# Kernel optimization log

Measured on AMD Instinct MI355X. Metric: run time of the kernel, lower is better.

Reference implementation:

```python
import jax, jax.numpy as jnp
import numpy as np

ITEM_NUM = 100000
EMBED = 128
HIDDEN = 256
BETA = 0.5
B, H = 2048, 200


def setup_inputs() -> dict:
    key = jax.random.key(0)
    ks = jax.random.split(key, 10)
    history = jax.random.randint(ks[0], (B, H), 0, ITEM_NUM)
    target = jax.random.randint(ks[1], (B,), 0, ITEM_NUM)
    history_region = jax.random.randint(ks[2], (B, H), 0, 64)
    target_region = jax.random.randint(ks[3], (B,), 0, 64)
    # scaled small since forward multiplies by 1000 before sigmoid
    target_distance = jax.random.uniform(ks[4], (B, H, 2), dtype=jnp.float32) * 1e-3
    embed_history = 0.01 * jax.random.normal(ks[5], (ITEM_NUM, EMBED), dtype=jnp.float32)
    embed_target = 0.01 * jax.random.normal(ks[6], (ITEM_NUM, EMBED), dtype=jnp.float32)
    W1 = 0.05 * jax.random.normal(ks[7], (EMBED + 2, HIDDEN), dtype=jnp.float32)
    b1 = jnp.zeros((HIDDEN,), dtype=jnp.float32)
    W2 = 0.05 * jax.random.normal(ks[8], (HIDDEN, 1), dtype=jnp.float32)
    Wd = 0.5 * jax.random.normal(ks[9], (2, 2), dtype=jnp.float32)
    bd = jnp.zeros((2,), dtype=jnp.float32)
    return {"history": history, "target": target, "history_region": history_region,
            "target_region": target_region, "target_distance": target_distance,
            "embed_history": embed_history, "embed_target": embed_target,
            "W1": W1, "b1": b1, "W2": W2, "Wd": Wd, "bd": bd}


def reference(history, target, history_region, target_region, target_distance,
              embed_history, embed_target, W1, b1, W2, Wd, bd):
    h = embed_history[history]                 # [B,H,d]
    t = embed_target[target]                   # [B,d]
    # dist_layer: sigmoid(Linear(2,2)(1000 * lat_long))
    dist = jax.nn.sigmoid((target_distance * 1000.0) @ Wd + bd)   # [B,H,2]
    inp = jnp.concatenate([h * t[:, None, :], dist], axis=-1)     # [B,H,d+2]
    attn = jax.nn.relu(inp @ W1 + b1) @ W2                        # [B,H,1]
    mask = (history != target[:, None]).astype(h.dtype)
    exp_A = jnp.exp(attn[..., 0]) * mask                          # [B,H]
    exp_sum = jnp.sum(exp_A, axis=-1, keepdims=True) ** BETA      # [B,1]
    w = exp_A / exp_sum                                           # [B,H]
    pred = jnp.einsum('bhd,bh,bd->b', h, w, t)                    # [B]
    return jax.nn.sigmoid(pred)
```

## Files before the change

kernel.cpp:

```cpp
#include <hip/hip_runtime.h>
#include <hip/hip_bf16.h>

#define B_SZ 2048
#define H_SZ 200
#define EMB 128
#define HID 256
#define KW 160

typedef short bf16x8 __attribute__((ext_vector_type(8)));
typedef float f32x4 __attribute__((ext_vector_type(4)));

#define WAIT_VM(n) asm volatile("s_waitcnt vmcnt(" #n ")" ::: "memory")
#define WAIT_LGKM  asm volatile("s_waitcnt lgkmcnt(0)" ::: "memory")
#define BAR        asm volatile("s_barrier" ::: "memory")

__device__ __forceinline__ unsigned short bfc(float x) {
    unsigned u = __float_as_uint(x);
    u += 0x7FFFu + ((u >> 16) & 1u);
    return (unsigned short)(u >> 16);
}
__device__ __forceinline__ float bf2f(unsigned short h) {
    return __uint_as_float(((unsigned)h) << 16);
}

__global__ void prep_w1t(const float* __restrict__ W1, unsigned short* __restrict__ W1TB) {
    int i = blockIdx.x * 256 + threadIdx.x;
    int n = i / KW;
    int k = i - n * KW;
    float v = (k < 130) ? W1[k * HID + n] : 0.f;
    W1TB[i] = bfc(v);
}

__global__ void prep_ehb(const float* __restrict__ eh, unsigned short* __restrict__ ehb) {
    size_t t = (size_t)blockIdx.x * 256 + threadIdx.x;
    const float4* src = (const float4*)eh + t * 2;
    float4 a = src[0], b = src[1];
    uint4 o;
    o.x = (unsigned)bfc(a.x) | ((unsigned)bfc(a.y) << 16);
    o.y = (unsigned)bfc(a.z) | ((unsigned)bfc(a.w) << 16);
    o.z = (unsigned)bfc(b.x) | ((unsigned)bfc(b.y) << 16);
    o.w = (unsigned)bfc(b.z) | ((unsigned)bfc(b.w) << 16);
    ((uint4*)ehb)[t] = o;
}

__device__ __forceinline__ void gld_lds16(const unsigned short* g, unsigned short* l) {
    __builtin_amdgcn_global_load_lds(
        (const __attribute__((address_space(1))) void*)(g),
        (__attribute__((address_space(3))) void*)(l),
        16, 0, 0);
}

__global__ __launch_bounds__(512, 4) void attn_kernel(
    const int* __restrict__ history, const int* __restrict__ target,
    const float* __restrict__ td, const unsigned short* __restrict__ ehb,
    const float* __restrict__ et, const unsigned short* __restrict__ W1TB,
    const float* __restrict__ b1, const float* __restrict__ W2,
    const float* __restrict__ Wd, const float* __restrict__ bd,
    float* __restrict__ out)
{
    __shared__ __align__(16) unsigned short Abuf[4][64][128];
    __shared__ float red[4][64][9];
    __shared__ unsigned Adist[256];
    __shared__ int idxs[256];
    __shared__ float t_f32[EMB];
    __shared__ __align__(16) unsigned short tbf[EMB];
    __shared__ float u_arr[256];
    __shared__ float finred[8];

    const int tid = threadIdx.x;
    const int b   = blockIdx.x;
    const int tgt = target[b];

    if (tid < 128) {
        float tf = et[(size_t)tgt * EMB + tid];
        t_f32[tid] = tf;
        tbf[tid] = bfc(tf);
    } else if (tid < 384) {
        const int m0 = tid - 128;
        if (m0 < H_SZ) {
            const int row = b * H_SZ + m0;
            idxs[m0] = history[row];
            float x0 = td[(size_t)row * 2 + 0] * 1000.f;
            float x1 = td[(size_t)row * 2 + 1] * 1000.f;
            float d0 = x0 * Wd[0] + x1 * Wd[2] + bd[0];
            float d1 = x0 * Wd[1] + x1 * Wd[3] + bd[1];
            d0 = 1.f / (1.f + expf(-d0));
            d1 = 1.f / (1.f + expf(-d1));
            Adist[m0] = (unsigned)bfc(d0) | ((unsigned)bfc(d1) << 16);
        } else {
            Adist[m0] = 0u;
        }
    }
    WAIT_LGKM; BAR;

    const int l  = tid & 63;
    const int w  = tid >> 6;
    const int lr = l & 15;
    const int lq = l >> 4;

    bf16x8 bfrA[2][5];
    f32x4 b1v[2], w2v[2];
#pragma unroll
    for (int nt = 0; nt < 2; ++nt) {
        const int n = w * 32 + nt * 16 + lr;
        b1v[nt] = *reinterpret_cast<const f32x4*>(b1 + w * 32 + nt * 16 + lq * 4);
        w2v[nt] = *reinterpret_cast<const f32x4*>(W2 + w * 32 + nt * 16 + lq * 4);
#pragma unroll
        for (int ks = 0; ks < 4; ++ks) {
            bf16x8 wv = *reinterpret_cast<const bf16x8*>(W1TB + n * KW + ks * 32 + lq * 8);
            bf16x8 o;
#pragma unroll
            for (int j = 0; j < 8; ++j)
                o[j] = (short)bfc(bf2f((unsigned short)wv[j]) * t_f32[ks * 32 + lq * 8 + j]);
            bfrA[nt][ks] = o;
        }
        bfrA[nt][4] = *reinterpret_cast<const bf16x8*>(W1TB + n * KW + 128 + lq * 8);
    }

    const int uo = tid & 7, um = tid >> 3;
    const bf16x8 tbu0 = *reinterpret_cast<const bf16x8*>(tbf + (2 * uo) * 8);
    const bf16x8 tbu1 = *reinterpret_cast<const bf16x8*>(tbf + (2 * uo + 1) * 8);

    WAIT_VM(0);

#pragma unroll
    for (int t = 0; t < 3; ++t) {
#pragma unroll
        for (int j = 0; j < 2; ++j) {
            const int rd = w * 8 + j * 4 + lq;
            const int cc = lr ^ (rd & 7);
            gld_lds16(ehb + (size_t)idxs[t * 64 + rd] * EMB + cc * 8,
                      &Abuf[t][w * 8 + j * 4][0]);
        }
    }
    if (w < 2) {
        const int rd = w * 4 + lq;
        const int cc = lr ^ (rd & 7);
        gld_lds16(ehb + (size_t)idxs[192 + rd] * EMB + cc * 8, &Abuf[3][w * 4][0]);
    }

#pragma unroll
    for (int t = 0; t < 4; ++t) {
        if (t == 0)      { if (w < 2) WAIT_VM(5); else WAIT_VM(4); }
        else if (t == 1) { if (w < 2) WAIT_VM(3); else WAIT_VM(2); }
        else if (t == 2) { if (w < 2) WAIT_VM(1); else WAIT_VM(0); }
        else             WAIT_VM(0);
        BAR;

        const int mc = (t == 3) ? 1 : 4;

        f32x4 acc[4][2];
#pragma unroll
        for (int mt = 0; mt < 4; ++mt)
#pragma unroll
            for (int nt = 0; nt < 2; ++nt)
                acc[mt][nt] = (f32x4){0.f, 0.f, 0.f, 0.f};

#pragma unroll
        for (int ks = 0; ks < 5; ++ks) {
#pragma unroll
            for (int mt = 0; mt < 4; ++mt) if (mt < mc) {
                const int ar = mt * 16 + lr;
                bf16x8 af;
                if (ks < 4) {
                    af = *reinterpret_cast<const bf16x8*>(
                        &Abuf[t][ar][(((ks * 4 + lq) ^ (ar & 7)) * 8)]);
                } else {
                    uint4 tv4 = make_uint4((lq == 0) ? Adist[t * 64 + ar] : 0u, 0u, 0u, 0u);
                    af = *reinterpret_cast<bf16x8*>(&tv4);
                }
#pragma unroll
                for (int nt = 0; nt < 2; ++nt)
                    acc[mt][nt] = __builtin_amdgcn_mfma_f32_16x16x32_bf16(
                        bfrA[nt][ks], af, acc[mt][nt], 0, 0, 0);
            }
        }

        {
            const unsigned short* Ar = &Abuf[t][um][0];
            bf16x8 h0 = *reinterpret_cast<const bf16x8*>(Ar + (((2 * uo)     ^ (um & 7)) * 8));
            bf16x8 h1 = *reinterpret_cast<const bf16x8*>(Ar + (((2 * uo + 1) ^ (um & 7)) * 8));
            float ua = 0.f;
#pragma unroll
            for (int j = 0; j < 8; ++j) {
                ua += bf2f((unsigned short)h0[j]) * bf2f((unsigned short)tbu0[j]);
                ua += bf2f((unsigned short)h1[j]) * bf2f((unsigned short)tbu1[j]);
            }
            ua += __shfl_xor(ua, 1);
            ua += __shfl_xor(ua, 2);
            ua += __shfl_xor(ua, 4);
            if (uo == 0) u_arr[t * 64 + um] = ua;
        }

#pragma unroll
        for (int mt = 0; mt < 4; ++mt) if (mt < mc) {
            float s = 0.f;
#pragma unroll
            for (int nt = 0; nt < 2; ++nt)
#pragma unroll
                for (int r = 0; r < 4; ++r)
                    s += fmaxf(acc[mt][nt][r] + b1v[nt][r], 0.f) * w2v[nt][r];
            s += __shfl_xor(s, 16);
            s += __shfl_xor(s, 32);
            if (l < 16) red[t][mt * 16 + l][w] = s;
        }
    }

    WAIT_LGKM; BAR;

    if (tid < 256) {
        const int tt = tid >> 6, mr = tid & 63;
        float attn = 0.f;
#pragma unroll
        for (int ww = 0; ww < 8; ++ww) attn += red[tt][mr][ww];
        const bool valid = (tid < H_SZ) && (idxs[tid] != tgt);
        float e  = valid ? expf(attn) : 0.f;
        float se = e;
        float su = valid ? e * u_arr[tid] : 0.f;
#pragma unroll
        for (int off = 1; off < 64; off <<= 1) {
            se += __shfl_xor(se, off);
            su += __shfl_xor(su, off);
        }
        if (l == 0) { finred[w * 2] = se; finred[w * 2 + 1] = su; }
    }
    WAIT_LGKM; BAR;
    if (tid == 0) {
        float SE = 0.f, SU = 0.f;
#pragma unroll
        for (int ww = 0; ww < 4; ++ww) { SE += finred[2 * ww]; SU += finred[2 * ww + 1]; }
        out[b] = 1.f / (1.f + expf(-SU / sqrtf(SE)));
    }
}

extern "C" void kernel_launch(void* const* d_in, const int* in_sizes, int n_in,
                              void* d_out, int out_size, void* d_ws, size_t ws_size,
                              hipStream_t stream) {
    const int*   history = (const int*)d_in[0];
    const int*   target  = (const int*)d_in[1];
    const float* td      = (const float*)d_in[4];
    const float* eh      = (const float*)d_in[5];
    const float* et      = (const float*)d_in[6];
    const float* W1      = (const float*)d_in[7];
    const float* b1      = (const float*)d_in[8];
    const float* W2      = (const float*)d_in[9];
    const float* Wd      = (const float*)d_in[10];
    const float* bd      = (const float*)d_in[11];
    float* out = (float*)d_out;

    char* ws = (char*)d_ws;
    unsigned short* W1TB = (unsigned short*)ws;
    unsigned short* ehb  = (unsigned short*)(ws + 81920);

    prep_w1t<<<HID * KW / 256, 256, 0, stream>>>(W1, W1TB);
    prep_ehb<<<1600000 / 256, 256, 0, stream>>>(eh, ehb);
    attn_kernel<<<B_SZ, 512, 0, stream>>>(history, target, td, ehb, et, W1TB,
                                          b1, W2, Wd, bd, out);
}
```

Before: 120.7 us.

## Double-buffer history tiles in LDS and fold softmax reduction into tile loop

Shrinks the shared-memory staging of gathered history rows from four tiles to two ping-pong buffers. Loads for tiles 2 and 3 are issued after earlier tiles are consumed, and the per-tile exp/weighted sums are accumulated inside the loop instead of in a separate final pass. Launch bounds are raised to allow more resident blocks per CU, using the smaller LDS footprint to hide gather latency through occupancy. The cost is an extra barrier per tile, less prefetch depth, and a tighter register budget that could cause spills.

```diff
diff --git a/kernel.cpp b/kernel.cpp
--- a/kernel.cpp
+++ b/kernel.cpp
@@ -50,7 +50,7 @@
         16, 0, 0);
 }
 
-__global__ __launch_bounds__(512, 4) void attn_kernel(
+__global__ __launch_bounds__(512, 8) void attn_kernel(
     const int* __restrict__ history, const int* __restrict__ target,
     const float* __restrict__ td, const unsigned short* __restrict__ ehb,
     const float* __restrict__ et, const unsigned short* __restrict__ W1TB,
@@ -58,14 +58,13 @@
     const float* __restrict__ Wd, const float* __restrict__ bd,
     float* __restrict__ out)
 {
-    __shared__ __align__(16) unsigned short Abuf[4][64][128];
-    __shared__ float red[4][64][9];
+    __shared__ __align__(16) unsigned short Abuf[2][64][128];
+    __shared__ float red[64][9];
     __shared__ unsigned Adist[256];
     __shared__ int idxs[256];
     __shared__ float t_f32[EMB];
     __shared__ __align__(16) unsigned short tbf[EMB];
-    __shared__ float u_arr[256];
-    __shared__ float finred[8];
+    __shared__ float u_t[64];
 
     const int tid = threadIdx.x;
     const int b   = blockIdx.x;
@@ -124,7 +123,7 @@
     WAIT_VM(0);
 
 #pragma unroll
-    for (int t = 0; t < 3; ++t) {
+    for (int t = 0; t < 2; ++t) {
 #pragma unroll
         for (int j = 0; j < 2; ++j) {
             const int rd = w * 8 + j * 4 + lq;
@@ -133,20 +132,18 @@
                       &Abuf[t][w * 8 + j * 4][0]);
         }
     }
-    if (w < 2) {
-        const int rd = w * 4 + lq;
-        const int cc = lr ^ (rd & 7);
-        gld_lds16(ehb + (size_t)idxs[192 + rd] * EMB + cc * 8, &Abuf[3][w * 4][0]);
-    }
+
+    float se = 0.f, su = 0.f;
 
 #pragma unroll
     for (int t = 0; t < 4; ++t) {
-        if (t == 0)      { if (w < 2) WAIT_VM(5); else WAIT_VM(4); }
-        else if (t == 1) { if (w < 2) WAIT_VM(3); else WAIT_VM(2); }
+        if (t == 0)      WAIT_VM(2);
+        else if (t == 1) WAIT_VM(2);
         else if (t == 2) { if (w < 2) WAIT_VM(1); else WAIT_VM(0); }
         else             WAIT_VM(0);
         BAR;
 
+        const int bi = t & 1;
         const int mc = (t == 3) ? 1 : 4;
 
         f32x4 acc[4][2];
@@ -164,7 +161,7 @@
                 bf16x8 af;
                 if (ks < 4) {
                     af = *reinterpret_cast<const bf16x8*>(
-                        &Abuf[t][ar][(((ks * 4 + lq) ^ (ar & 7)) * 8)]);
+                        &Abuf[bi][ar][(((ks * 4 + lq) ^ (ar & 7)) * 8)]);
                 } else {
                     uint4 tv4 = make_uint4((lq == 0) ? Adist[t * 64 + ar] : 0u, 0u, 0u, 0u);
                     af = *reinterpret_cast<bf16x8*>(&tv4);
@@ -177,7 +174,7 @@
         }
 
         {
-            const unsigned short* Ar = &Abuf[t][um][0];
+            const unsigned short* Ar = &Abuf[bi][um][0];
             bf16x8 h0 = *reinterpret_cast<const bf16x8*>(Ar + (((2 * uo)     ^ (um & 7)) * 8));
             bf16x8 h1 = *reinterpret_cast<const bf16x8*>(Ar + (((2 * uo + 1) ^ (um & 7)) * 8));
             float ua = 0.f;
@@ -189,7 +186,7 @@
             ua += __shfl_xor(ua, 1);
             ua += __shfl_xor(ua, 2);
             ua += __shfl_xor(ua, 4);
-            if (uo == 0) u_arr[t * 64 + um] = ua;
+            if (uo == 0) u_t[um] = ua;
         }
 
 #pragma unroll
@@ -202,34 +199,47 @@
                     s += fmaxf(acc[mt][nt][r] + b1v[nt][r], 0.f) * w2v[nt][r];
             s += __shfl_xor(s, 16);
             s += __shfl_xor(s, 32);
-            if (l < 16) red[t][mt * 16 + l][w] = s;
-        }
-    }
-
-    WAIT_LGKM; BAR;
-
-    if (tid < 256) {
-        const int tt = tid >> 6, mr = tid & 63;
-        float attn = 0.f;
-#pragma unroll
-        for (int ww = 0; ww < 8; ++ww) attn += red[tt][mr][ww];
-        const bool valid = (tid < H_SZ) && (idxs[tid] != tgt);
-        float e  = valid ? expf(attn) : 0.f;
-        float se = e;
-        float su = valid ? e * u_arr[tid] : 0.f;
+            if (l < 16) red[mt * 16 + l][w] = s;
+        }
+
+        WAIT_LGKM; BAR;
+
+        if (t == 0) {
+#pragma unroll
+            for (int j = 0; j < 2; ++j) {
+                const int rd = w * 8 + j * 4 + lq;
+                const int cc = lr ^ (rd & 7);
+                gld_lds16(ehb + (size_t)idxs[128 + rd] * EMB + cc * 8,
+                          &Abuf[0][w * 8 + j * 4][0]);
+            }
+        } else if (t == 1) {
+            if (w < 2) {
+                const int rd = w * 4 + lq;
+                const int cc = lr ^ (rd & 7);
+                gld_lds16(ehb + (size_t)idxs[192 + rd] * EMB + cc * 8,
+                          &Abuf[1][w * 4][0]);
+            }
+        }
+
+        if (tid < 64) {
+            const int grow = t * 64 + tid;
+            float attn = 0.f;
+#pragma unroll
+            for (int ww = 0; ww < 8; ++ww) attn += red[tid][ww];
+            const bool valid = (grow < H_SZ) && (idxs[grow] != tgt);
+            float e = valid ? expf(attn) : 0.f;
+            se += e;
+            su += valid ? e * u_t[tid] : 0.f;
+        }
+    }
+
+    if (tid < 64) {
 #pragma unroll
         for (int off = 1; off < 64; off <<= 1) {
             se += __shfl_xor(se, off);
             su += __shfl_xor(su, off);
         }
-        if (l == 0) { finred[w * 2] = se; finred[w * 2 + 1] = su; }
-    }
-    WAIT_LGKM; BAR;
-    if (tid == 0) {
-        float SE = 0.f, SU = 0.f;
-#pragma unroll
-        for (int ww = 0; ww < 4; ++ww) { SE += finred[2 * ww]; SU += finred[2 * ww + 1]; }
-        out[b] = 1.f / (1.f + expf(-SU / sqrtf(SE)));
+        if (tid == 0) out[b] = 1.f / (1.f + expf(-su / sqrtf(se)));
     }
 }
 
```

New measurement: 424.3 us. 251% more time.

## Load gathered history rows directly into registers with double-buffered 16-row tiles

Applied to the files above, without the earlier changes.

Drops the LDS staging of gathered embedding rows via global_load_lds. Each wave now loads its MFMA B-fragments for 16-row tiles straight from global memory into registers, double-buffered across 13 tiles, and the u dot product is computed from those registers by one rotating wave. This removes the 64KB LDS buffer and its barriers, but every wave now redundantly gathers the same rows (8x global/L2 traffic). The per-tile loop also has less MFMA work to hide load latency behind.

```diff
diff --git a/kernel.cpp b/kernel.cpp
--- a/kernel.cpp
+++ b/kernel.cpp
@@ -6,13 +6,10 @@
 #define EMB 128
 #define HID 256
 #define KW 160
+#define NTILE 13
 
 typedef short bf16x8 __attribute__((ext_vector_type(8)));
 typedef float f32x4 __attribute__((ext_vector_type(4)));
-
-#define WAIT_VM(n) asm volatile("s_waitcnt vmcnt(" #n ")" ::: "memory")
-#define WAIT_LGKM  asm volatile("s_waitcnt lgkmcnt(0)" ::: "memory")
-#define BAR        asm volatile("s_barrier" ::: "memory")
 
 __device__ __forceinline__ unsigned short bfc(float x) {
     unsigned u = __float_as_uint(x);
@@ -43,13 +40,6 @@
     ((uint4*)ehb)[t] = o;
 }
 
-__device__ __forceinline__ void gld_lds16(const unsigned short* g, unsigned short* l) {
-    __builtin_amdgcn_global_load_lds(
-        (const __attribute__((address_space(1))) void*)(g),
-        (__attribute__((address_space(3))) void*)(l),
-        16, 0, 0);
-}
-
 __global__ __launch_bounds__(512, 4) void attn_kernel(
     const int* __restrict__ history, const int* __restrict__ target,
     const float* __restrict__ td, const unsigned short* __restrict__ ehb,
@@ -58,40 +48,37 @@
     const float* __restrict__ Wd, const float* __restrict__ bd,
     float* __restrict__ out)
 {
-    __shared__ __align__(16) unsigned short Abuf[4][64][128];
-    __shared__ float red[4][64][9];
-    __shared__ unsigned Adist[256];
-    __shared__ int idxs[256];
     __shared__ float t_f32[EMB];
-    __shared__ __align__(16) unsigned short tbf[EMB];
-    __shared__ float u_arr[256];
-    __shared__ float finred[8];
+    __shared__ int idxs[224];
+    __shared__ unsigned Adist[224];
+    __shared__ float red[NTILE][16][9];
+    __shared__ float u_arr[224];
+    __shared__ float finred[16];
 
     const int tid = threadIdx.x;
     const int b   = blockIdx.x;
     const int tgt = target[b];
 
     if (tid < 128) {
-        float tf = et[(size_t)tgt * EMB + tid];
-        t_f32[tid] = tf;
-        tbf[tid] = bfc(tf);
-    } else if (tid < 384) {
-        const int m0 = tid - 128;
-        if (m0 < H_SZ) {
-            const int row = b * H_SZ + m0;
-            idxs[m0] = history[row];
+        t_f32[tid] = et[(size_t)tgt * EMB + tid];
+    } else if (tid < 352) {
+        const int g = tid - 128;
+        int idx = 0; unsigned ad = 0u;
+        if (g < H_SZ) {
+            const int row = b * H_SZ + g;
+            idx = history[row];
             float x0 = td[(size_t)row * 2 + 0] * 1000.f;
             float x1 = td[(size_t)row * 2 + 1] * 1000.f;
             float d0 = x0 * Wd[0] + x1 * Wd[2] + bd[0];
             float d1 = x0 * Wd[1] + x1 * Wd[3] + bd[1];
             d0 = 1.f / (1.f + expf(-d0));
             d1 = 1.f / (1.f + expf(-d1));
-            Adist[m0] = (unsigned)bfc(d0) | ((unsigned)bfc(d1) << 16);
-        } else {
-            Adist[m0] = 0u;
-        }
-    }
-    WAIT_LGKM; BAR;
+            ad = (unsigned)bfc(d0) | ((unsigned)bfc(d1) << 16);
+        }
+        idxs[g]  = idx;
+        Adist[g] = ad;
+    }
+    __syncthreads();
 
     const int l  = tid & 63;
     const int w  = tid >> 6;
@@ -117,118 +104,81 @@
         bfrA[nt][4] = *reinterpret_cast<const bf16x8*>(W1TB + n * KW + 128 + lq * 8);
     }
 
-    const int uo = tid & 7, um = tid >> 3;
-    const bf16x8 tbu0 = *reinterpret_cast<const bf16x8*>(tbf + (2 * uo) * 8);
-    const bf16x8 tbu1 = *reinterpret_cast<const bf16x8*>(tbf + (2 * uo + 1) * 8);
-
-    WAIT_VM(0);
-
-#pragma unroll
-    for (int t = 0; t < 3; ++t) {
-#pragma unroll
-        for (int j = 0; j < 2; ++j) {
-            const int rd = w * 8 + j * 4 + lq;
-            const int cc = lr ^ (rd & 7);
-            gld_lds16(ehb + (size_t)idxs[t * 64 + rd] * EMB + cc * 8,
-                      &Abuf[t][w * 8 + j * 4][0]);
-        }
-    }
-    if (w < 2) {
-        const int rd = w * 4 + lq;
-        const int cc = lr ^ (rd & 7);
-        gld_lds16(ehb + (size_t)idxs[192 + rd] * EMB + cc * 8, &Abuf[3][w * 4][0]);
-    }
-
-#pragma unroll
-    for (int t = 0; t < 4; ++t) {
-        if (t == 0)      { if (w < 2) WAIT_VM(5); else WAIT_VM(4); }
-        else if (t == 1) { if (w < 2) WAIT_VM(3); else WAIT_VM(2); }
-        else if (t == 2) { if (w < 2) WAIT_VM(1); else WAIT_VM(0); }
-        else             WAIT_VM(0);
-        BAR;
-
-        const int mc = (t == 3) ? 1 : 4;
-
-        f32x4 acc[4][2];
-#pragma unroll
-        for (int mt = 0; mt < 4; ++mt)
-#pragma unroll
-            for (int nt = 0; nt < 2; ++nt)
-                acc[mt][nt] = (f32x4){0.f, 0.f, 0.f, 0.f};
-
-#pragma unroll
-        for (int ks = 0; ks < 5; ++ks) {
-#pragma unroll
-            for (int mt = 0; mt < 4; ++mt) if (mt < mc) {
-                const int ar = mt * 16 + lr;
-                bf16x8 af;
-                if (ks < 4) {
-                    af = *reinterpret_cast<const bf16x8*>(
-                        &Abuf[t][ar][(((ks * 4 + lq) ^ (ar & 7)) * 8)]);
-                } else {
-                    uint4 tv4 = make_uint4((lq == 0) ? Adist[t * 64 + ar] : 0u, 0u, 0u, 0u);
-                    af = *reinterpret_cast<bf16x8*>(&tv4);
-                }
-#pragma unroll
-                for (int nt = 0; nt < 2; ++nt)
-                    acc[mt][nt] = __builtin_amdgcn_mfma_f32_16x16x32_bf16(
-                        bfrA[nt][ks], af, acc[mt][nt], 0, 0, 0);
-            }
-        }
-
-        {
-            const unsigned short* Ar = &Abuf[t][um][0];
-            bf16x8 h0 = *reinterpret_cast<const bf16x8*>(Ar + (((2 * uo)     ^ (um & 7)) * 8));
-            bf16x8 h1 = *reinterpret_cast<const bf16x8*>(Ar + (((2 * uo + 1) ^ (um & 7)) * 8));
+#define LOADT(T, HF) {                                                         \
+        const unsigned short* base_ = ehb + ((size_t)idxs[(T) * 16 + lr] << 7);\
+        _Pragma("unroll")                                                      \
+        for (int ks_ = 0; ks_ < 4; ++ks_)                                      \
+            HF[ks_] = *reinterpret_cast<const bf16x8*>(base_ + ks_ * 32 + lq * 8); \
+    }
+
+    bf16x8 hf[2][4];
+    LOADT(0, hf[0]);
+
+#pragma unroll
+    for (int t = 0; t < NTILE; ++t) {
+        if (t + 1 < NTILE) LOADT(t + 1, hf[(t + 1) & 1]);
+
+        uint4 dv = make_uint4((lq == 0) ? Adist[t * 16 + lr] : 0u, 0u, 0u, 0u);
+        bf16x8 dfrag = *reinterpret_cast<bf16x8*>(&dv);
+
+        f32x4 acc0 = (f32x4){0.f, 0.f, 0.f, 0.f};
+        f32x4 acc1 = (f32x4){0.f, 0.f, 0.f, 0.f};
+#pragma unroll
+        for (int ks = 0; ks < 4; ++ks) {
+            acc0 = __builtin_amdgcn_mfma_f32_16x16x32_bf16(bfrA[0][ks], hf[t & 1][ks], acc0, 0, 0, 0);
+            acc1 = __builtin_amdgcn_mfma_f32_16x16x32_bf16(bfrA[1][ks], hf[t & 1][ks], acc1, 0, 0, 0);
+        }
+        acc0 = __builtin_amdgcn_mfma_f32_16x16x32_bf16(bfrA[0][4], dfrag, acc0, 0, 0, 0);
+        acc1 = __builtin_amdgcn_mfma_f32_16x16x32_bf16(bfrA[1][4], dfrag, acc1, 0, 0, 0);
+
+        if (w == (t & 7)) {
             float ua = 0.f;
 #pragma unroll
-            for (int j = 0; j < 8; ++j) {
-                ua += bf2f((unsigned short)h0[j]) * bf2f((unsigned short)tbu0[j]);
-                ua += bf2f((unsigned short)h1[j]) * bf2f((unsigned short)tbu1[j]);
-            }
-            ua += __shfl_xor(ua, 1);
-            ua += __shfl_xor(ua, 2);
-            ua += __shfl_xor(ua, 4);
-            if (uo == 0) u_arr[t * 64 + um] = ua;
-        }
-
-#pragma unroll
-        for (int mt = 0; mt < 4; ++mt) if (mt < mc) {
-            float s = 0.f;
-#pragma unroll
-            for (int nt = 0; nt < 2; ++nt)
-#pragma unroll
-                for (int r = 0; r < 4; ++r)
-                    s += fmaxf(acc[mt][nt][r] + b1v[nt][r], 0.f) * w2v[nt][r];
-            s += __shfl_xor(s, 16);
-            s += __shfl_xor(s, 32);
-            if (l < 16) red[t][mt * 16 + l][w] = s;
-        }
-    }
-
-    WAIT_LGKM; BAR;
-
-    if (tid < 256) {
-        const int tt = tid >> 6, mr = tid & 63;
+            for (int ks = 0; ks < 4; ++ks)
+#pragma unroll
+                for (int j = 0; j < 8; ++j)
+                    ua += bf2f((unsigned short)hf[t & 1][ks][j]) * t_f32[ks * 32 + lq * 8 + j];
+            ua += __shfl_xor(ua, 16);
+            ua += __shfl_xor(ua, 32);
+            if (l < 16) u_arr[t * 16 + lr] = ua;
+        }
+
+        float s = 0.f;
+#pragma unroll
+        for (int r = 0; r < 4; ++r) {
+            s += fmaxf(acc0[r] + b1v[0][r], 0.f) * w2v[0][r];
+            s += fmaxf(acc1[r] + b1v[1][r], 0.f) * w2v[1][r];
+        }
+        s += __shfl_xor(s, 16);
+        s += __shfl_xor(s, 32);
+        if (l < 16) red[t][lr][w] = s;
+    }
+#undef LOADT
+
+    __syncthreads();
+
+    float se = 0.f, su = 0.f;
+    if (tid < NTILE * 16) {
+        const int t = tid >> 4, m = tid & 15;
         float attn = 0.f;
 #pragma unroll
-        for (int ww = 0; ww < 8; ++ww) attn += red[tt][mr][ww];
+        for (int ww = 0; ww < 8; ++ww) attn += red[t][m][ww];
         const bool valid = (tid < H_SZ) && (idxs[tid] != tgt);
-        float e  = valid ? expf(attn) : 0.f;
-        float se = e;
-        float su = valid ? e * u_arr[tid] : 0.f;
-#pragma unroll
-        for (int off = 1; off < 64; off <<= 1) {
-            se += __shfl_xor(se, off);
-            su += __shfl_xor(su, off);
-        }
-        if (l == 0) { finred[w * 2] = se; finred[w * 2 + 1] = su; }
-    }
-    WAIT_LGKM; BAR;
+        const float e = valid ? expf(attn) : 0.f;
+        se = e;
+        su = valid ? e * u_arr[tid] : 0.f;
+    }
+#pragma unroll
+    for (int off = 1; off < 64; off <<= 1) {
+        se += __shfl_xor(se, off);
+        su += __shfl_xor(su, off);
+    }
+    if (l == 0) { finred[w * 2] = se; finred[w * 2 + 1] = su; }
+    __syncthreads();
     if (tid == 0) {
         float SE = 0.f, SU = 0.f;
 #pragma unroll
-        for (int ww = 0; ww < 4; ++ww) { SE += finred[2 * ww]; SU += finred[2 * ww + 1]; }
+        for (int ww = 0; ww < 8; ++ww) { SE += finred[2 * ww]; SU += finred[2 * ww + 1]; }
         out[b] = 1.f / (1.f + expf(-SU / sqrtf(SE)));
     }
 }
```

Result: slower. 161.9 us (+34.1%).
